# Performance work log

Hardware: AMD Instinct MI355X
Metric: run time of the kernel (lower is better)

## Reference

```python
import jax, jax.numpy as jnp
import numpy as np

N_HEADS = 8
HEAD_DIM = 64


def setup_inputs() -> dict:
    key = jax.random.key(0)
    ks = jax.random.split(key, 5)
    B, L, D = 2, 2048, 512
    Dh = N_HEADS * HEAD_DIM  # 512
    scale_init = 0.02
    return {
        "x": jax.random.normal(ks[0], (B, L, D), dtype=jnp.float32),
        "wq": jax.random.normal(ks[1], (D, Dh), dtype=jnp.float32) * scale_init,
        "wk": jax.random.normal(ks[2], (D, Dh), dtype=jnp.float32) * scale_init,
        "wv": jax.random.normal(ks[3], (D, Dh), dtype=jnp.float32) * scale_init,
        "wo": jax.random.normal(ks[4], (Dh, D), dtype=jnp.float32) * scale_init,
    }


def reference(x, wq, wk, wv, wo):
    B, L, D = x.shape
    H, Dh = N_HEADS, HEAD_DIM
    scale = 1.0 / (Dh ** 0.5)

    q = (x @ wq).reshape(B, L, H, Dh)
    k = (x @ wk).reshape(B, L, H, Dh)
    v = (x @ wv).reshape(B, L, H, Dh)

    # [B, H, L, S] scores; diagonal (token attending to itself) is masked out.
    scores = jnp.einsum('blhe,bshe->bhls', q, k) * scale
    diag = jnp.eye(L, dtype=bool)  # [L, L]
    scores = jnp.where(diag, -jnp.inf, scores)
    attn = jax.nn.softmax(scores, axis=-1)

    out = jnp.einsum('bhls,bshd->blhd', attn, v).reshape(B, L, H * Dh)
    return out @ wo
```

## Files before the change

### kernel.cpp

```cpp
#include <hip/hip_runtime.h>
#include <hip/hip_bf16.h>
#include <math.h>

typedef __bf16 bf16;
typedef __bf16 bf16x8 __attribute__((ext_vector_type(8)));
typedef float f32x4 __attribute__((ext_vector_type(4)));

#define AS1 __attribute__((address_space(1)))
#define AS3 __attribute__((address_space(3)))

__device__ __forceinline__ void gload_lds16(const void* g, void* l) {
  __builtin_amdgcn_global_load_lds((const AS1 void*)g, (AS3 void*)l, 16, 0, 0);
}

__global__ __launch_bounds__(256) void cvt_x_kernel(const float* __restrict__ x,
                                                    bf16* __restrict__ xb) {
  int i = (blockIdx.x * 256 + threadIdx.x) * 8;
  float4 a = *(const float4*)(x + i);
  float4 b = *(const float4*)(x + i + 4);
  bf16x8 o;
  o[0] = (bf16)a.x; o[1] = (bf16)a.y; o[2] = (bf16)a.z; o[3] = (bf16)a.w;
  o[4] = (bf16)b.x; o[5] = (bf16)b.y; o[6] = (bf16)b.z; o[7] = (bf16)b.w;
  *(bf16x8*)(xb + i) = o;
}

__global__ __launch_bounds__(256) void transpose_w_kernel(
    const float* __restrict__ wq, const float* __restrict__ wk,
    const float* __restrict__ wv, const float* __restrict__ wo,
    bf16* __restrict__ wqkv_t, bf16* __restrict__ wo_t) {
  __shared__ float t[64 * 65];
  int ct = blockIdx.x & 31, kt = blockIdx.x >> 5;
  int p = ct >> 3;
  const float* src = (p == 0) ? wq : (p == 1) ? wk : (p == 2) ? wv : wo;
  int c0 = (ct & 7) * 64;
  int k0 = kt * 64;
  int tid = threadIdx.x;
  for (int i = 0; i < 16; ++i) {
    int idx = i * 256 + tid;
    int r = idx >> 6, c = idx & 63;
    t[r * 65 + c] = src[(size_t)(k0 + r) * 512 + c0 + c];
  }
  __syncthreads();
  for (int i = 0; i < 16; ++i) {
    int idx = i * 256 + tid;
    int cc = idx >> 6, kk = idx & 63;
    float v = t[kk * 65 + cc];
    int col = c0 + cc;
    if (p < 3) wqkv_t[(size_t)(p * 512 + col) * 512 + k0 + kk] = (bf16)v;
    else       wo_t[(size_t)col * 512 + k0 + kk] = (bf16)v;
  }
}

template <int MODE, int BM, int BN>
__global__ __launch_bounds__(256) void gemm_kernel(
    const bf16* __restrict__ A, const bf16* __restrict__ Bt,
    float* __restrict__ Cf, bf16* __restrict__ qw, bf16* __restrict__ kw,
    bf16* __restrict__ vtw, int M, int N, int K) {
  __shared__ bf16 ldsA[BM * 64];
  __shared__ bf16 ldsB[BN * 64];
  constexpr int MF = BM / 32;
  constexpr int NF = BN / 32;
  int tid = threadIdx.x;
  int wave = tid >> 6, l = tid & 63;
  int lr = l & 15, lg = l >> 4;
  int nbm = M / BM;
  int bm = blockIdx.x % nbm, bn = blockIdx.x / nbm;
  int wr = wave >> 1, wc = wave & 1;

  f32x4 acc[MF][NF] = {};

  for (int k0 = 0; k0 < K; k0 += 64) {
    #pragma unroll
    for (int i = 0; i < BM * 128 / 4096; ++i) {
      int off = i * 4096 + tid * 16;
      int r = off >> 7, cb = off & 127;
      gload_lds16((const char*)(A + (size_t)(bm * BM + r) * K + k0) + cb,
                  (char*)ldsA + i * 4096 + wave * 1024);
    }
    #pragma unroll
    for (int i = 0; i < BN * 128 / 4096; ++i) {
      int off = i * 4096 + tid * 16;
      int r = off >> 7, cb = off & 127;
      gload_lds16((const char*)(Bt + (size_t)(bn * BN + r) * K + k0) + cb,
                  (char*)ldsB + i * 4096 + wave * 1024);
    }
    __syncthreads();
    #pragma unroll
    for (int ks = 0; ks < 2; ++ks) {
      bf16x8 af[MF], bfr[NF];
      #pragma unroll
      for (int m = 0; m < MF; ++m)
        af[m] = *(const bf16x8*)(ldsA + (wr * (BM / 2) + m * 16 + lr) * 64 + ks * 32 + lg * 8);
      #pragma unroll
      for (int n = 0; n < NF; ++n)
        bfr[n] = *(const bf16x8*)(ldsB + (wc * (BN / 2) + n * 16 + lr) * 64 + ks * 32 + lg * 8);
      #pragma unroll
      for (int m = 0; m < MF; ++m)
        #pragma unroll
        for (int n = 0; n < NF; ++n)
          acc[m][n] = __builtin_amdgcn_mfma_f32_16x16x32_bf16(af[m], bfr[n], acc[m][n], 0, 0, 0);
    }
    __syncthreads();
  }

  #pragma unroll
  for (int m = 0; m < MF; ++m)
    #pragma unroll
    for (int n = 0; n < NF; ++n)
      #pragma unroll
      for (int j = 0; j < 4; ++j) {
        float v = acc[m][n][j];
        int row = bm * BM + wr * (BM / 2) + m * 16 + lg * 4 + j;
        int col = bn * BN + wc * (BN / 2) + n * 16 + lr;
        if (MODE == 1) {
          Cf[(size_t)row * N + col] = v;
        } else {
          int part = col >> 9, cp = col & 511;
          int h = cp >> 6, d = cp & 63;
          int b = row >> 11, lq = row & 2047;
          size_t bh = (size_t)(b * 8 + h);
          if (part == 0)      qw[(bh * 2048 + lq) * 64 + d] = (bf16)(v * 0.18033688f);
          else if (part == 1) kw[(bh * 2048 + lq) * 64 + d] = (bf16)v;
          else                vtw[(bh * 64 + d) * 2048 + lq] = (bf16)v;
        }
      }
}

__global__ __launch_bounds__(512, 4) void attn_kernel(
    const bf16* __restrict__ qw, const bf16* __restrict__ kw,
    const bf16* __restrict__ vtw,
    bf16* __restrict__ pO0, bf16* __restrict__ pO1,
    bf16* __restrict__ pO2, bf16* __restrict__ pO3,
    float* __restrict__ pL0, float* __restrict__ pL1,
    float* __restrict__ pL2, float* __restrict__ pL3) {
  __shared__ bf16 ldsK[2][64 * 64];
  __shared__ bf16 ldsV[2][64 * 64];
  __shared__ bf16 ldsP[8][2][16 * 64];

  int swzb = ((blockIdx.x & 7) << 6) | (blockIdx.x >> 3);
  int qblk = swzb & 7, kv = (swzb >> 3) & 3, bh = swzb >> 5;

  int tid = threadIdx.x, wave = tid >> 6, l = tid & 63;
  int lr = l & 15, lg = l >> 4;
  const bf16* Q  = qw  + (size_t)bh * 2048 * 64;
  const bf16* Kp = kw  + (size_t)bh * 2048 * 64;
  const bf16* Vt = vtw + (size_t)bh * 64 * 2048;
  int q0 = qblk * 256;
  int td = qblk * 4 + (wave >> 1);
  int qrelA = (wave & 1) * 32;
  int qrelB = qrelA + 16;

  bf16x8 qfA[2], qfB[2];
  #pragma unroll
  for (int ks = 0; ks < 2; ++ks) {
    qfA[ks] = *(const bf16x8*)(Q + (size_t)(q0 + wave * 32 + lr) * 64 + ks * 32 + lg * 8);
    qfB[ks] = *(const bf16x8*)(Q + (size_t)(q0 + wave * 32 + 16 + lr) * 64 + ks * 32 + lg * 8);
  }

  int rowT = tid >> 3;
  int colT = (tid * 16) & 127;
  int swzcol = colT ^ ((rowT & 7) << 4);
  int swzk = rowT * 128 + swzcol;
  size_t vsrc = (size_t)rowT * 4096 + swzcol;

  f32x4 accA[4] = {}, accB[4] = {};
  float lA[4] = {0.f, 0.f, 0.f, 0.f}, lB[4] = {0.f, 0.f, 0.f, 0.f};

  auto stage = [&](int buf, int t) {
    gload_lds16((const char*)Kp + (size_t)t * 8192 + swzk, (char*)ldsK[buf] + wave * 1024);
    gload_lds16((const char*)Vt + (size_t)t * 128 + vsrc,  (char*)ldsV[buf] + wave * 1024);
  };

  int t0 = kv * 8;
  stage(0, t0);

  int rxor = (lr & 7) << 4;

  for (int tt = 0; tt < 8; ++tt) {
    int t = t0 + tt;
    int buf = tt & 1;
    if (tt < 7) {
      stage(buf ^ 1, t + 1);
      asm volatile("s_waitcnt vmcnt(2)" ::: "memory");
    } else {
      asm volatile("s_waitcnt vmcnt(0)" ::: "memory");
    }
    __builtin_amdgcn_s_barrier();
    __builtin_amdgcn_sched_barrier(0);

    f32x4 saA[4] = {}, saB[4] = {};
    __builtin_amdgcn_s_setprio(1);
    #pragma unroll
    for (int ks = 0; ks < 2; ++ks) {
      #pragma unroll
      for (int n = 0; n < 4; ++n) {
        bf16x8 kf = *(const bf16x8*)((const char*)ldsK[buf] + (n * 16 + lr) * 128 +
                                     ((ks * 64 + lg * 16) ^ rxor));
        saA[n] = __builtin_amdgcn_mfma_f32_16x16x32_bf16(qfA[ks], kf, saA[n], 0, 0, 0);
        saB[n] = __builtin_amdgcn_mfma_f32_16x16x32_bf16(qfB[ks], kf, saB[n], 0, 0, 0);
      }
    }
    __builtin_amdgcn_s_setprio(0);

    if (t == td) {
      #pragma unroll
      for (int n = 0; n < 4; ++n)
        #pragma unroll
        for (int j = 0; j < 4; ++j) {
          if (n * 16 + lr == qrelA + lg * 4 + j) saA[n][j] = -INFINITY;
          if (n * 16 + lr == qrelB + lg * 4 + j) saB[n][j] = -INFINITY;
        }
    }

    char* PA = (char*)ldsP[wave][0];
    char* PB = (char*)ldsP[wave][1];
    #pragma unroll
    for (int n = 0; n < 4; ++n)
      #pragma unroll
      for (int j = 0; j < 4; ++j) {
        int rowP = lg * 4 + j;
        int cswz = ((n * 16 + lr) * 2) ^ ((rowP & 7) << 4);
        float pA = exp2f(saA[n][j]);
        lA[j] += pA;
        *(bf16*)(PA + rowP * 128 + cswz) = (bf16)pA;
        float pB = exp2f(saB[n][j]);
        lB[j] += pB;
        *(bf16*)(PB + rowP * 128 + cswz) = (bf16)pB;
      }

    __builtin_amdgcn_s_setprio(1);
    #pragma unroll
    for (int ks = 0; ks < 2; ++ks) {
      bf16x8 pfA = *(const bf16x8*)(PA + lr * 128 + ((ks * 64 + lg * 16) ^ rxor));
      bf16x8 pfB = *(const bf16x8*)(PB + lr * 128 + ((ks * 64 + lg * 16) ^ rxor));
      #pragma unroll
      for (int n = 0; n < 4; ++n) {
        bf16x8 vf = *(const bf16x8*)((const char*)ldsV[buf] + (n * 16 + lr) * 128 +
                                     ((ks * 64 + lg * 16) ^ rxor));
        accA[n] = __builtin_amdgcn_mfma_f32_16x16x32_bf16(pfA, vf, accA[n], 0, 0, 0);
        accB[n] = __builtin_amdgcn_mfma_f32_16x16x32_bf16(pfB, vf, accB[n], 0, 0, 0);
      }
    }
    __builtin_amdgcn_s_setprio(0);
    __builtin_amdgcn_s_barrier();
  }

  #pragma unroll
  for (int j = 0; j < 4; ++j)
    #pragma unroll
    for (int dd = 1; dd < 16; dd <<= 1) {
      lA[j] += __shfl_xor(lA[j], dd);
      lB[j] += __shfl_xor(lB[j], dd);
    }

  bf16*  pO = (kv == 0) ? pO0 : (kv == 1) ? pO1 : (kv == 2) ? pO2 : pO3;
  float* pL = (kv == 0) ? pL0 : (kv == 1) ? pL1 : (kv == 2) ? pL2 : pL3;
  #pragma unroll
  for (int j = 0; j < 4; ++j) {
    int gqA = q0 + wave * 32 + lg * 4 + j;
    int gqB = gqA + 16;
    if (lr == 0) {
      pL[(size_t)bh * 2048 + gqA] = lA[j];
      pL[(size_t)bh * 2048 + gqB] = lB[j];
    }
    #pragma unroll
    for (int n = 0; n < 4; ++n) {
      pO[((size_t)bh * 2048 + gqA) * 64 + n * 16 + lr] = (bf16)accA[n][j];
      pO[((size_t)bh * 2048 + gqB) * 64 + n * 16 + lr] = (bf16)accB[n][j];
    }
  }
}

__global__ __launch_bounds__(256) void combine_kernel(
    const bf16* __restrict__ pO0, const bf16* __restrict__ pO1,
    const bf16* __restrict__ pO2, const bf16* __restrict__ pO3,
    const float* __restrict__ pL0, const float* __restrict__ pL1,
    const float* __restrict__ pL2, const float* __restrict__ pL3,
    bf16* __restrict__ ao) {
  int idx = blockIdx.x * 256 + threadIdx.x;
  int e8 = idx * 8;
  int row = e8 >> 9, col = e8 & 511;
  int b = row >> 11, lq = row & 2047, h = col >> 6, d0 = col & 63;
  size_t bhq = (size_t)(b * 8 + h) * 2048 + lq;
  size_t src = bhq * 64 + d0;
  bf16x8 v0 = *(const bf16x8*)(pO0 + src);
  bf16x8 v1 = *(const bf16x8*)(pO1 + src);
  bf16x8 v2 = *(const bf16x8*)(pO2 + src);
  bf16x8 v3 = *(const bf16x8*)(pO3 + src);
  float inv = 1.f / (pL0[bhq] + pL1[bhq] + pL2[bhq] + pL3[bhq]);
  bf16x8 o;
  #pragma unroll
  for (int i = 0; i < 8; ++i)
    o[i] = (bf16)(((float)v0[i] + (float)v1[i] + (float)v2[i] + (float)v3[i]) * inv);
  *(bf16x8*)(ao + e8) = o;
}

extern "C" void kernel_launch(void* const* d_in, const int* in_sizes, int n_in,
                              void* d_out, int out_size, void* d_ws, size_t ws_size,
                              hipStream_t stream) {
  const float* x  = (const float*)d_in[0];
  const float* wq = (const float*)d_in[1];
  const float* wk = (const float*)d_in[2];
  const float* wv = (const float*)d_in[3];
  const float* wo = (const float*)d_in[4];

  if (ws_size < (32u << 20)) return;

  char* ws = (char*)d_ws;
  bf16* xb     = (bf16*)(ws);
  bf16* wqkv_t = (bf16*)(ws + (4 << 20));
  bf16* wo_t   = (bf16*)(ws + (6 << 20));
  bf16* q_ws   = (bf16*)(ws + (8 << 20));
  bf16* k_ws   = (bf16*)(ws + (12 << 20));
  bf16* vt_ws  = (bf16*)(ws + (16 << 20));
  bf16*  pO0 = (bf16*)(ws);
  float* pL0 = (float*)(ws + (4 << 20));
  float* pL1 = (float*)(ws + (4 << 20) + (128 << 10));
  float* pL2 = (float*)(ws + (4 << 20) + (256 << 10));
  float* pL3 = (float*)(ws + (4 << 20) + (384 << 10));
  bf16*  pO1 = (bf16*)(ws + (20 << 20));
  bf16*  pO2 = (bf16*)(ws + (24 << 20));
  bf16*  pO3 = (bf16*)(ws + (28 << 20));
  bf16*  ao  = (bf16*)(ws + (8 << 20));

  cvt_x_kernel<<<1024, 256, 0, stream>>>(x, xb);
  transpose_w_kernel<<<256, 256, 0, stream>>>(wq, wk, wv, wo, wqkv_t, wo_t);
  gemm_kernel<0, 64, 128><<<64 * 12, 256, 0, stream>>>(xb, wqkv_t, nullptr, q_ws, k_ws,
                                                       vt_ws, 4096, 1536, 512);
  attn_kernel<<<512, 512, 0, stream>>>(q_ws, k_ws, vt_ws, pO0, pO1, pO2, pO3,
                                       pL0, pL1, pL2, pL3);
  combine_kernel<<<1024, 256, 0, stream>>>(pO0, pO1, pO2, pO3, pL0, pL1, pL2, pL3, ao);
  gemm_kernel<1, 64, 64><<<64 * 8, 256, 0, stream>>>(ao, wo_t, (float*)d_out, nullptr,
                                                     nullptr, nullptr, 4096, 512, 512);
}
```

Before: 82.22 us.

## Fuse x conversion into QKV GEMM and split-KV combine into output GEMM

The standalone fp32-to-bf16 conversion of x is removed: the QKV GEMM now loads fp32 x directly, converts it and writes it to LDS. The combine kernel that merged the four split-KV partial outputs is folded into the output projection's A-tile load, so the intermediate attention-output buffer is never written or re-read. This drops two kernel launches and their global round trips. The cost is that partials and x are re-read once per N-tile and that LDS stores now wait on synchronous loads instead of async global-to-LDS copies. The attention kernel's launch-bounds occupancy hint also changes from 4 to 3.

After: 92.11 us. 1.12x slower.

```diff
diff --git a/kernel.cpp b/kernel.cpp
--- a/kernel.cpp
+++ b/kernel.cpp
@@ -3,6 +3,7 @@
 #include <math.h>
 
 typedef __bf16 bf16;
+typedef __bf16 bf16x4 __attribute__((ext_vector_type(4)));
 typedef __bf16 bf16x8 __attribute__((ext_vector_type(8)));
 typedef float f32x4 __attribute__((ext_vector_type(4)));
 
@@ -11,17 +12,6 @@
 
 __device__ __forceinline__ void gload_lds16(const void* g, void* l) {
   __builtin_amdgcn_global_load_lds((const AS1 void*)g, (AS3 void*)l, 16, 0, 0);
-}
-
-__global__ __launch_bounds__(256) void cvt_x_kernel(const float* __restrict__ x,
-                                                    bf16* __restrict__ xb) {
-  int i = (blockIdx.x * 256 + threadIdx.x) * 8;
-  float4 a = *(const float4*)(x + i);
-  float4 b = *(const float4*)(x + i + 4);
-  bf16x8 o;
-  o[0] = (bf16)a.x; o[1] = (bf16)a.y; o[2] = (bf16)a.z; o[3] = (bf16)a.w;
-  o[4] = (bf16)b.x; o[5] = (bf16)b.y; o[6] = (bf16)b.z; o[7] = (bf16)b.w;
-  *(bf16x8*)(xb + i) = o;
 }
 
 __global__ __launch_bounds__(256) void transpose_w_kernel(
@@ -51,82 +41,75 @@
   }
 }
 
-template <int MODE, int BM, int BN>
-__global__ __launch_bounds__(256) void gemm_kernel(
-    const bf16* __restrict__ A, const bf16* __restrict__ Bt,
-    float* __restrict__ Cf, bf16* __restrict__ qw, bf16* __restrict__ kw,
-    bf16* __restrict__ vtw, int M, int N, int K) {
-  __shared__ bf16 ldsA[BM * 64];
-  __shared__ bf16 ldsB[BN * 64];
-  constexpr int MF = BM / 32;
-  constexpr int NF = BN / 32;
+__global__ __launch_bounds__(256) void gemm_qkv_kernel(
+    const float* __restrict__ x, const bf16* __restrict__ Bt,
+    bf16* __restrict__ qw, bf16* __restrict__ kw, bf16* __restrict__ vtw) {
+  __shared__ bf16 ldsA[64 * 64];
+  __shared__ bf16 ldsB[128 * 64];
   int tid = threadIdx.x;
   int wave = tid >> 6, l = tid & 63;
   int lr = l & 15, lg = l >> 4;
-  int nbm = M / BM;
-  int bm = blockIdx.x % nbm, bn = blockIdx.x / nbm;
+  int bm = blockIdx.x & 63, bn = blockIdx.x >> 6;
   int wr = wave >> 1, wc = wave & 1;
 
-  f32x4 acc[MF][NF] = {};
-
-  for (int k0 = 0; k0 < K; k0 += 64) {
-    #pragma unroll
-    for (int i = 0; i < BM * 128 / 4096; ++i) {
+  f32x4 acc[2][4] = {};
+
+  for (int k0 = 0; k0 < 512; k0 += 64) {
+    #pragma unroll
+    for (int i = 0; i < 4; ++i) {
       int off = i * 4096 + tid * 16;
       int r = off >> 7, cb = off & 127;
-      gload_lds16((const char*)(A + (size_t)(bm * BM + r) * K + k0) + cb,
-                  (char*)ldsA + i * 4096 + wave * 1024);
-    }
-    #pragma unroll
-    for (int i = 0; i < BN * 128 / 4096; ++i) {
-      int off = i * 4096 + tid * 16;
-      int r = off >> 7, cb = off & 127;
-      gload_lds16((const char*)(Bt + (size_t)(bn * BN + r) * K + k0) + cb,
+      gload_lds16((const char*)(Bt + (size_t)(bn * 128 + r) * 512 + k0) + cb,
                   (char*)ldsB + i * 4096 + wave * 1024);
     }
+    #pragma unroll
+    for (int c = 0; c < 4; ++c) {
+      int idx = c * 256 + tid;
+      int r = idx >> 4, f4 = idx & 15;
+      float4 v = *(const float4*)(x + (size_t)(bm * 64 + r) * 512 + k0 + f4 * 4);
+      bf16x4 o;
+      o[0] = (bf16)v.x; o[1] = (bf16)v.y; o[2] = (bf16)v.z; o[3] = (bf16)v.w;
+      *(bf16x4*)(ldsA + r * 64 + f4 * 4) = o;
+    }
     __syncthreads();
     #pragma unroll
     for (int ks = 0; ks < 2; ++ks) {
-      bf16x8 af[MF], bfr[NF];
-      #pragma unroll
-      for (int m = 0; m < MF; ++m)
-        af[m] = *(const bf16x8*)(ldsA + (wr * (BM / 2) + m * 16 + lr) * 64 + ks * 32 + lg * 8);
-      #pragma unroll
-      for (int n = 0; n < NF; ++n)
-        bfr[n] = *(const bf16x8*)(ldsB + (wc * (BN / 2) + n * 16 + lr) * 64 + ks * 32 + lg * 8);
-      #pragma unroll
-      for (int m = 0; m < MF; ++m)
+      bf16x8 af[2], bfr[4];
+      #pragma unroll
+      for (int m = 0; m < 2; ++m)
+        af[m] = *(const bf16x8*)(ldsA + (wr * 32 + m * 16 + lr) * 64 + ks * 32 + lg * 8);
+      #pragma unroll
+      for (int n = 0; n < 4; ++n)
+        bfr[n] = *(const bf16x8*)(ldsB + (wc * 64 + n * 16 + lr) * 64 + ks * 32 + lg * 8);
+      #pragma unroll
+      for (int m = 0; m < 2; ++m)
         #pragma unroll
-        for (int n = 0; n < NF; ++n)
+        for (int n = 0; n < 4; ++n)
           acc[m][n] = __builtin_amdgcn_mfma_f32_16x16x32_bf16(af[m], bfr[n], acc[m][n], 0, 0, 0);
     }
     __syncthreads();
   }
 
   #pragma unroll
-  for (int m = 0; m < MF; ++m)
-    #pragma unroll
-    for (int n = 0; n < NF; ++n)
+  for (int m = 0; m < 2; ++m)
+    #pragma unroll
+    for (int n = 0; n < 4; ++n)
       #pragma unroll
       for (int j = 0; j < 4; ++j) {
         float v = acc[m][n][j];
-        int row = bm * BM + wr * (BM / 2) + m * 16 + lg * 4 + j;
-        int col = bn * BN + wc * (BN / 2) + n * 16 + lr;
-        if (MODE == 1) {
-          Cf[(size_t)row * N + col] = v;
-        } else {
-          int part = col >> 9, cp = col & 511;
-          int h = cp >> 6, d = cp & 63;
-          int b = row >> 11, lq = row & 2047;
-          size_t bh = (size_t)(b * 8 + h);
-          if (part == 0)      qw[(bh * 2048 + lq) * 64 + d] = (bf16)(v * 0.18033688f);
-          else if (part == 1) kw[(bh * 2048 + lq) * 64 + d] = (bf16)v;
-          else                vtw[(bh * 64 + d) * 2048 + lq] = (bf16)v;
-        }
-      }
-}
-
-__global__ __launch_bounds__(512, 4) void attn_kernel(
+        int row = bm * 64 + wr * 32 + m * 16 + lg * 4 + j;
+        int col = bn * 128 + wc * 64 + n * 16 + lr;
+        int part = col >> 9, cp = col & 511;
+        int h = cp >> 6, d = cp & 63;
+        int b = row >> 11, lq = row & 2047;
+        size_t bh = (size_t)(b * 8 + h);
+        if (part == 0)      qw[(bh * 2048 + lq) * 64 + d] = (bf16)(v * 0.18033688f);
+        else if (part == 1) kw[(bh * 2048 + lq) * 64 + d] = (bf16)v;
+        else                vtw[(bh * 64 + d) * 2048 + lq] = (bf16)v;
+      }
+}
+
+__global__ __launch_bounds__(512, 3) void attn_kernel(
     const bf16* __restrict__ qw, const bf16* __restrict__ kw,
     const bf16* __restrict__ vtw,
     bf16* __restrict__ pO0, bf16* __restrict__ pO1,
@@ -271,28 +254,79 @@
   }
 }
 
-__global__ __launch_bounds__(256) void combine_kernel(
+__global__ __launch_bounds__(256) void gemm_out_kernel(
     const bf16* __restrict__ pO0, const bf16* __restrict__ pO1,
     const bf16* __restrict__ pO2, const bf16* __restrict__ pO3,
     const float* __restrict__ pL0, const float* __restrict__ pL1,
     const float* __restrict__ pL2, const float* __restrict__ pL3,
-    bf16* __restrict__ ao) {
-  int idx = blockIdx.x * 256 + threadIdx.x;
-  int e8 = idx * 8;
-  int row = e8 >> 9, col = e8 & 511;
-  int b = row >> 11, lq = row & 2047, h = col >> 6, d0 = col & 63;
-  size_t bhq = (size_t)(b * 8 + h) * 2048 + lq;
-  size_t src = bhq * 64 + d0;
-  bf16x8 v0 = *(const bf16x8*)(pO0 + src);
-  bf16x8 v1 = *(const bf16x8*)(pO1 + src);
-  bf16x8 v2 = *(const bf16x8*)(pO2 + src);
-  bf16x8 v3 = *(const bf16x8*)(pO3 + src);
-  float inv = 1.f / (pL0[bhq] + pL1[bhq] + pL2[bhq] + pL3[bhq]);
-  bf16x8 o;
-  #pragma unroll
-  for (int i = 0; i < 8; ++i)
-    o[i] = (bf16)(((float)v0[i] + (float)v1[i] + (float)v2[i] + (float)v3[i]) * inv);
-  *(bf16x8*)(ao + e8) = o;
+    const bf16* __restrict__ Bt, float* __restrict__ Cf) {
+  __shared__ bf16 ldsA[64 * 64];
+  __shared__ bf16 ldsB[64 * 64];
+  int tid = threadIdx.x;
+  int wave = tid >> 6, l = tid & 63;
+  int lr = l & 15, lg = l >> 4;
+  int bm = blockIdx.x & 63, bn = blockIdx.x >> 6;
+  int wr = wave >> 1, wc = wave & 1;
+
+  f32x4 acc[2][2] = {};
+
+  for (int k0 = 0; k0 < 512; k0 += 64) {
+    int h = k0 >> 6;
+    #pragma unroll
+    for (int i = 0; i < 2; ++i) {
+      int off = i * 4096 + tid * 16;
+      int r = off >> 7, cb = off & 127;
+      gload_lds16((const char*)(Bt + (size_t)(bn * 64 + r) * 512 + k0) + cb,
+                  (char*)ldsB + i * 4096 + wave * 1024);
+    }
+    #pragma unroll
+    for (int i = 0; i < 2; ++i) {
+      int off = i * 4096 + tid * 16;
+      int r = off >> 7, d0 = (off & 127) >> 1;
+      int rg = bm * 64 + r;
+      int b = rg >> 11, lq = rg & 2047;
+      size_t bhq = ((size_t)(b * 8 + h)) * 2048 + lq;
+      size_t src = bhq * 64 + d0;
+      bf16x8 v0 = *(const bf16x8*)(pO0 + src);
+      bf16x8 v1 = *(const bf16x8*)(pO1 + src);
+      bf16x8 v2 = *(const bf16x8*)(pO2 + src);
+      bf16x8 v3 = *(const bf16x8*)(pO3 + src);
+      float inv = 1.f / (pL0[bhq] + pL1[bhq] + pL2[bhq] + pL3[bhq]);
+      bf16x8 o;
+      #pragma unroll
+      for (int e = 0; e < 8; ++e)
+        o[e] = (bf16)(((float)v0[e] + (float)v1[e] + (float)v2[e] + (float)v3[e]) * inv);
+      *(bf16x8*)(ldsA + r * 64 + d0) = o;
+    }
+    __syncthreads();
+    #pragma unroll
+    for (int ks = 0; ks < 2; ++ks) {
+      bf16x8 af[2], bfr[2];
+      #pragma unroll
+      for (int m = 0; m < 2; ++m)
+        af[m] = *(const bf16x8*)(ldsA + (wr * 32 + m * 16 + lr) * 64 + ks * 32 + lg * 8);
+      #pragma unroll
+      for (int n = 0; n < 2; ++n)
+        bfr[n] = *(const bf16x8*)(ldsB + (wc * 32 + n * 16 + lr) * 64 + ks * 32 + lg * 8);
+      #pragma unroll
+      for (int m = 0; m < 2; ++m)
+        #pragma unroll
+        for (int n = 0; n < 2; ++n)
+          acc[m][n] = __builtin_amdgcn_mfma_f32_16x16x32_bf16(af[m], bfr[n], acc[m][n], 0, 0, 0);
+    }
+    __syncthreads();
+  }
+
+  #pragma unroll
+  for (int m = 0; m < 2; ++m)
+    #pragma unroll
+    for (int n = 0; n < 2; ++n)
+      #pragma unroll
+      for (int j = 0; j < 4; ++j) {
+        int row = bm * 64 + wr * 32 + m * 16 + lg * 4 + j;
+        int col = bn * 64 + wc * 32 + n * 16 + lr;
+        Cf[(size_t)row * 512 + col] = acc[m][n][j];
+      }
 }
 
 extern "C" void kernel_launch(void* const* d_in, const int* in_sizes, int n_in,
@@ -307,7 +341,6 @@
   if (ws_size < (32u << 20)) return;
 
   char* ws = (char*)d_ws;
-  bf16* xb     = (bf16*)(ws);
   bf16* wqkv_t = (bf16*)(ws + (4 << 20));
   bf16* wo_t   = (bf16*)(ws + (6 << 20));
   bf16* q_ws   = (bf16*)(ws + (8 << 20));
@@ -321,15 +354,11 @@
   bf16*  pO1 = (bf16*)(ws + (20 << 20));
   bf16*  pO2 = (bf16*)(ws + (24 << 20));
   bf16*  pO3 = (bf16*)(ws + (28 << 20));
-  bf16*  ao  = (bf16*)(ws + (8 << 20));
-
-  cvt_x_kernel<<<1024, 256, 0, stream>>>(x, xb);
+
   transpose_w_kernel<<<256, 256, 0, stream>>>(wq, wk, wv, wo, wqkv_t, wo_t);
-  gemm_kernel<0, 64, 128><<<64 * 12, 256, 0, stream>>>(xb, wqkv_t, nullptr, q_ws, k_ws,
-                                                       vt_ws, 4096, 1536, 512);
+  gemm_qkv_kernel<<<64 * 12, 256, 0, stream>>>(x, wqkv_t, q_ws, k_ws, vt_ws);
   attn_kernel<<<512, 512, 0, stream>>>(q_ws, k_ws, vt_ws, pO0, pO1, pO2, pO3,
                                        pL0, pL1, pL2, pL3);
-  combine_kernel<<<1024, 256, 0, stream>>>(pO0, pO1, pO2, pO3, pL0, pL1, pL2, pL3, ao);
-  gemm_kernel<1, 64, 64><<<64 * 8, 256, 0, stream>>>(ao, wo_t, (float*)d_out, nullptr,
-                                                     nullptr, nullptr, 4096, 512, 512);
-}
+  gemm_out_kernel<<<512, 256, 0, stream>>>(pO0, pO1, pO2, pO3, pL0, pL1, pL2, pL3,
+                                           wo_t, (float*)d_out);
+}
```

## Compute transposed scores so P stays in registers and widen per-wave query tile

Applied to the files above, without the earlier changes.

The attention kernel now computes S^T = K·Q^T, which leaves the probabilities in a register layout that can be fed straight into the P·V MFMA. This removes the per-wave LDS round trip for P. Each wave now handles 64 query rows instead of 32, so every K/V fragment read from LDS is reused across four MFMAs. The grid halves to 256 blocks with launch bounds of two blocks per CU, and the K/V swizzle and row permutation are changed to match the new fragment layout. In exchange it needs more accumulator registers, and with fewer blocks the GPU's CUs may not all be filled.

After: 80.96 us. Within noise of the previous version (-1.5%).

```diff
diff --git a/kernel.cpp b/kernel.cpp
--- a/kernel.cpp
+++ b/kernel.cpp
@@ -5,12 +5,21 @@
 typedef __bf16 bf16;
 typedef __bf16 bf16x8 __attribute__((ext_vector_type(8)));
 typedef float f32x4 __attribute__((ext_vector_type(4)));
+typedef unsigned int uint32x4 __attribute__((ext_vector_type(4)));
 
 #define AS1 __attribute__((address_space(1)))
 #define AS3 __attribute__((address_space(3)))
 
 __device__ __forceinline__ void gload_lds16(const void* g, void* l) {
   __builtin_amdgcn_global_load_lds((const AS1 void*)g, (AS3 void*)l, 16, 0, 0);
+}
+
+__device__ __forceinline__ unsigned packbf16(float a, float b) {
+  bf16 x = (bf16)a, y = (bf16)b;
+  unsigned short ux, uy;
+  __builtin_memcpy(&ux, &x, 2);
+  __builtin_memcpy(&uy, &y, 2);
+  return (unsigned)ux | ((unsigned)uy << 16);
 }
 
 __global__ __launch_bounds__(256) void cvt_x_kernel(const float* __restrict__ x,
@@ -126,7 +135,7 @@
       }
 }
 
-__global__ __launch_bounds__(512, 4) void attn_kernel(
+__global__ __launch_bounds__(512, 2) void attn_kernel(
     const bf16* __restrict__ qw, const bf16* __restrict__ kw,
     const bf16* __restrict__ vtw,
     bf16* __restrict__ pO0, bf16* __restrict__ pO1,
@@ -135,46 +144,44 @@
     float* __restrict__ pL2, float* __restrict__ pL3) {
   __shared__ bf16 ldsK[2][64 * 64];
   __shared__ bf16 ldsV[2][64 * 64];
-  __shared__ bf16 ldsP[8][2][16 * 64];
-
-  int swzb = ((blockIdx.x & 7) << 6) | (blockIdx.x >> 3);
-  int qblk = swzb & 7, kv = (swzb >> 3) & 3, bh = swzb >> 5;
+
+  int swzb = ((blockIdx.x & 7) << 5) | (blockIdx.x >> 3);
+  int bh = swzb >> 4, kv = swzb & 3, qblk = (swzb >> 2) & 3;
 
   int tid = threadIdx.x, wave = tid >> 6, l = tid & 63;
   int lr = l & 15, lg = l >> 4;
   const bf16* Q  = qw  + (size_t)bh * 2048 * 64;
   const bf16* Kp = kw  + (size_t)bh * 2048 * 64;
   const bf16* Vt = vtw + (size_t)bh * 64 * 2048;
-  int q0 = qblk * 256;
-  int td = qblk * 4 + (wave >> 1);
-  int qrelA = (wave & 1) * 32;
-  int qrelB = qrelA + 16;
-
-  bf16x8 qfA[2], qfB[2];
-  #pragma unroll
-  for (int ks = 0; ks < 2; ++ks) {
-    qfA[ks] = *(const bf16x8*)(Q + (size_t)(q0 + wave * 32 + lr) * 64 + ks * 32 + lg * 8);
-    qfB[ks] = *(const bf16x8*)(Q + (size_t)(q0 + wave * 32 + 16 + lr) * 64 + ks * 32 + lg * 8);
-  }
+  int qbase = qblk * 512 + wave * 64;
+  int td = qblk * 8 + wave;
+
+  bf16x8 qf[4][2];
+  #pragma unroll
+  for (int s = 0; s < 4; ++s)
+    #pragma unroll
+    for (int ks = 0; ks < 2; ++ks)
+      qf[s][ks] = *(const bf16x8*)(Q + (size_t)(qbase + s * 16 + lr) * 64 + ks * 32 + lg * 8);
 
   int rowT = tid >> 3;
-  int colT = (tid * 16) & 127;
-  int swzcol = colT ^ ((rowT & 7) << 4);
-  int swzk = rowT * 128 + swzcol;
-  size_t vsrc = (size_t)rowT * 4096 + swzcol;
-
-  f32x4 accA[4] = {}, accB[4] = {};
-  float lA[4] = {0.f, 0.f, 0.f, 0.f}, lB[4] = {0.f, 0.f, 0.f, 0.f};
+  int colT = (tid & 7) * 16;
+  int swc = colT ^ ((((rowT & 3) | (((rowT >> 3) & 1) << 2))) << 4);
+
+  int kxor = (((lr & 3) | (((lr >> 2) & 1) << 2)) << 4);
+  int vxor = (((lr & 3) | (((lr >> 3) & 1) << 2)) << 4);
+
+  f32x4 acc[4][4] = {};
+  float lsum[4] = {0.f, 0.f, 0.f, 0.f};
 
   auto stage = [&](int buf, int t) {
-    gload_lds16((const char*)Kp + (size_t)t * 8192 + swzk, (char*)ldsK[buf] + wave * 1024);
-    gload_lds16((const char*)Vt + (size_t)t * 128 + vsrc,  (char*)ldsV[buf] + wave * 1024);
+    gload_lds16((const char*)Kp + (size_t)t * 8192 + rowT * 128 + swc,
+                (char*)ldsK[buf] + wave * 1024);
+    gload_lds16((const char*)Vt + (size_t)t * 128 + (size_t)rowT * 4096 + swc,
+                (char*)ldsV[buf] + wave * 1024);
   };
 
   int t0 = kv * 8;
   stage(0, t0);
-
-  int rxor = (lr & 7) << 4;
 
   for (int tt = 0; tt < 8; ++tt) {
     int t = t0 + tt;
@@ -188,85 +195,85 @@
     __builtin_amdgcn_s_barrier();
     __builtin_amdgcn_sched_barrier(0);
 
-    f32x4 saA[4] = {}, saB[4] = {};
+    f32x4 ps[4][4] = {};
     __builtin_amdgcn_s_setprio(1);
     #pragma unroll
-    for (int ks = 0; ks < 2; ++ks) {
+    for (int ks = 0; ks < 2; ++ks)
       #pragma unroll
       for (int n = 0; n < 4; ++n) {
-        bf16x8 kf = *(const bf16x8*)((const char*)ldsK[buf] + (n * 16 + lr) * 128 +
-                                     ((ks * 64 + lg * 16) ^ rxor));
-        saA[n] = __builtin_amdgcn_mfma_f32_16x16x32_bf16(qfA[ks], kf, saA[n], 0, 0, 0);
-        saB[n] = __builtin_amdgcn_mfma_f32_16x16x32_bf16(qfB[ks], kf, saB[n], 0, 0, 0);
+        int mrow = ((n >> 1) << 5) + ((lr >> 2) << 3) + ((n & 1) << 2) + (lr & 3);
+        bf16x8 kf = *(const bf16x8*)((const char*)ldsK[buf] + mrow * 128 +
+                                     ((ks * 64 + lg * 16) ^ kxor));
+        #pragma unroll
+        for (int s = 0; s < 4; ++s)
+          ps[s][n] = __builtin_amdgcn_mfma_f32_16x16x32_bf16(kf, qf[s][ks], ps[s][n], 0, 0, 0);
       }
-    }
     __builtin_amdgcn_s_setprio(0);
 
     if (t == td) {
       #pragma unroll
-      for (int n = 0; n < 4; ++n)
+      for (int s = 0; s < 4; ++s)
         #pragma unroll
-        for (int j = 0; j < 4; ++j) {
-          if (n * 16 + lr == qrelA + lg * 4 + j) saA[n][j] = -INFINITY;
-          if (n * 16 + lr == qrelB + lg * 4 + j) saB[n][j] = -INFINITY;
-        }
-    }
-
-    char* PA = (char*)ldsP[wave][0];
-    char* PB = (char*)ldsP[wave][1];
-    #pragma unroll
-    for (int n = 0; n < 4; ++n)
-      #pragma unroll
-      for (int j = 0; j < 4; ++j) {
-        int rowP = lg * 4 + j;
-        int cswz = ((n * 16 + lr) * 2) ^ ((rowP & 7) << 4);
-        float pA = exp2f(saA[n][j]);
-        lA[j] += pA;
-        *(bf16*)(PA + rowP * 128 + cswz) = (bf16)pA;
-        float pB = exp2f(saB[n][j]);
-        lB[j] += pB;
-        *(bf16*)(PB + rowP * 128 + cswz) = (bf16)pB;
+        for (int n = 0; n < 4; ++n)
+          #pragma unroll
+          for (int j = 0; j < 4; ++j)
+            if (((n >> 1) * 32 + lg * 8 + (n & 1) * 4 + j) == s * 16 + lr)
+              ps[s][n][j] = -INFINITY;
+    }
+
+    bf16x8 pf[4][2];
+    #pragma unroll
+    for (int s = 0; s < 4; ++s) {
+      unsigned u[4][2];
+      #pragma unroll
+      for (int n = 0; n < 4; ++n) {
+        float p0 = exp2f(ps[s][n][0]);
+        float p1 = exp2f(ps[s][n][1]);
+        float p2 = exp2f(ps[s][n][2]);
+        float p3 = exp2f(ps[s][n][3]);
+        lsum[s] += p0 + p1 + p2 + p3;
+        u[n][0] = packbf16(p0, p1);
+        u[n][1] = packbf16(p2, p3);
       }
+      uint32x4 w0 = {u[0][0], u[0][1], u[1][0], u[1][1]};
+      uint32x4 w1 = {u[2][0], u[2][1], u[3][0], u[3][1]};
+      pf[s][0] = __builtin_bit_cast(bf16x8, w0);
+      pf[s][1] = __builtin_bit_cast(bf16x8, w1);
+    }
 
     __builtin_amdgcn_s_setprio(1);
     #pragma unroll
-    for (int ks = 0; ks < 2; ++ks) {
-      bf16x8 pfA = *(const bf16x8*)(PA + lr * 128 + ((ks * 64 + lg * 16) ^ rxor));
-      bf16x8 pfB = *(const bf16x8*)(PB + lr * 128 + ((ks * 64 + lg * 16) ^ rxor));
+    for (int ks = 0; ks < 2; ++ks)
       #pragma unroll
       for (int n = 0; n < 4; ++n) {
-        bf16x8 vf = *(const bf16x8*)((const char*)ldsV[buf] + (n * 16 + lr) * 128 +
-                                     ((ks * 64 + lg * 16) ^ rxor));
-        accA[n] = __builtin_amdgcn_mfma_f32_16x16x32_bf16(pfA, vf, accA[n], 0, 0, 0);
-        accB[n] = __builtin_amdgcn_mfma_f32_16x16x32_bf16(pfB, vf, accB[n], 0, 0, 0);
+        int vrow = n * 16 + lr;
+        bf16x8 vf = *(const bf16x8*)((const char*)ldsV[buf] + vrow * 128 +
+                                     ((ks * 64 + lg * 16) ^ vxor));
+        #pragma unroll
+        for (int s = 0; s < 4; ++s)
+          acc[s][n] = __builtin_amdgcn_mfma_f32_16x16x32_bf16(pf[s][ks], vf, acc[s][n], 0, 0, 0);
       }
-    }
     __builtin_amdgcn_s_setprio(0);
     __builtin_amdgcn_s_barrier();
   }
 
   #pragma unroll
-  for (int j = 0; j < 4; ++j)
-    #pragma unroll
-    for (int dd = 1; dd < 16; dd <<= 1) {
-      lA[j] += __shfl_xor(lA[j], dd);
-      lB[j] += __shfl_xor(lB[j], dd);
-    }
+  for (int s = 0; s < 4; ++s) {
+    lsum[s] += __shfl_xor(lsum[s], 16);
+    lsum[s] += __shfl_xor(lsum[s], 32);
+  }
 
   bf16*  pO = (kv == 0) ? pO0 : (kv == 1) ? pO1 : (kv == 2) ? pO2 : pO3;
   float* pL = (kv == 0) ? pL0 : (kv == 1) ? pL1 : (kv == 2) ? pL2 : pL3;
   #pragma unroll
-  for (int j = 0; j < 4; ++j) {
-    int gqA = q0 + wave * 32 + lg * 4 + j;
-    int gqB = gqA + 16;
-    if (lr == 0) {
-      pL[(size_t)bh * 2048 + gqA] = lA[j];
-      pL[(size_t)bh * 2048 + gqB] = lB[j];
-    }
-    #pragma unroll
-    for (int n = 0; n < 4; ++n) {
-      pO[((size_t)bh * 2048 + gqA) * 64 + n * 16 + lr] = (bf16)accA[n][j];
-      pO[((size_t)bh * 2048 + gqB) * 64 + n * 16 + lr] = (bf16)accB[n][j];
+  for (int s = 0; s < 4; ++s) {
+    if (lg == 0) pL[(size_t)bh * 2048 + qbase + s * 16 + lr] = lsum[s];
+    #pragma unroll
+    for (int j = 0; j < 4; ++j) {
+      int gq = qbase + s * 16 + lg * 4 + j;
+      #pragma unroll
+      for (int n = 0; n < 4; ++n)
+        pO[((size_t)bh * 2048 + gq) * 64 + n * 16 + lr] = (bf16)acc[s][n][j];
     }
   }
 }
@@ -327,7 +334,7 @@
   transpose_w_kernel<<<256, 256, 0, stream>>>(wq, wk, wv, wo, wqkv_t, wo_t);
   gemm_kernel<0, 64, 128><<<64 * 12, 256, 0, stream>>>(xb, wqkv_t, nullptr, q_ws, k_ws,
                                                        vt_ws, 4096, 1536, 512);
-  attn_kernel<<<512, 512, 0, stream>>>(q_ws, k_ws, vt_ws, pO0, pO1, pO2, pO3,
+  attn_kernel<<<256, 512, 0, stream>>>(q_ws, k_ws, vt_ws, pO0, pO1, pO2, pO3,
                                        pL0, pL1, pL2, pL3);
   combine_kernel<<<1024, 256, 0, stream>>>(pO0, pO1, pO2, pO3, pL0, pL1, pL2, pL3, ao);
   gemm_kernel<1, 64, 64><<<64 * 8, 256, 0, stream>>>(ao, wo_t, (float*)d_out, nullptr,
```
